# Performance work log

Measured on AMD Instinct MI355X. Metric: run time of the kernel, lower is better.

The kernel has to match this reference:

```python
import jax, jax.numpy as jnp
import numpy as np

B, S, D, F, E = 1, 1024, 1024, 4096, 8  # batch, seq, embed_dim, ffn_dim, num_experts(workers)
EPS = 1e-5


def setup_inputs() -> dict:
    key = jax.random.key(0)
    ks = jax.random.split(key, 4)
    x = jax.random.normal(ks[0], (B, S, D), jnp.float32)
    # expert centroids (orthogonal init gain 0.1 in original; scaled normal is fine for a reference)
    centroids = jax.random.normal(ks[1], (E, D), jnp.float32) * 0.1
    # per-expert BaseSublayer params (LayerNorm + ff1 + ff2); torch Linear convention W:[out,in]
    gamma = jnp.ones((E, D), jnp.float32)
    beta = jnp.zeros((E, D), jnp.float32)
    W1 = jax.random.normal(ks[2], (E, F, D), jnp.float32) * 0.02
    b1 = jnp.zeros((E, F), jnp.float32)
    W2 = jax.random.normal(ks[3], (E, D, F), jnp.float32) * 0.02  # zero-init in original; random for testing
    b2 = jnp.zeros((E, D), jnp.float32)
    return {"x": x, "centroids": centroids, "gamma": gamma, "beta": beta,
            "W1": W1, "b1": b1, "W2": W2, "b2": b2}


def _sublayer(xs, g, b, W1e, b1e, W2e, b2e):
    # BaseSublayer: xs + ff2(relu(ff1(LN(xs))))
    mu = jnp.mean(xs, axis=-1, keepdims=True)
    var = jnp.mean(jnp.square(xs - mu), axis=-1, keepdims=True)
    h = (xs - mu) * jax.lax.rsqrt(var + EPS) * g + b
    return xs + jax.nn.relu(h @ W1e.T + b1e) @ W2e.T + b2e


def reference(x, centroids, gamma, beta, W1, b1, W2, b2):
    feats = x.reshape(-1, x.shape[-1])                      # [T, D]
    # affinity matmul is under torch.no_grad in the original -> stop_gradient
    scores = jax.lax.stop_gradient(feats @ centroids.T)     # [T, E]
    expert = jnp.argmax(scores, axis=1)                     # greedy top-1 assignment
    onehot = jax.nn.one_hot(expert, E, dtype=feats.dtype)   # [T, E]
    # sigmoid gate: alpha = sigmoid(x . centroid[expert(x)])
    alpha = jax.nn.sigmoid(jnp.sum(feats * centroids[expert], axis=-1, keepdims=True))
    # run each expert's sublayer over all tokens, combine by assignment (dense reference
    # for the sort/gather dispatch + scatter combine of the original)
    ys = jax.vmap(_sublayer, in_axes=(None, 0, 0, 0, 0, 0, 0))(
        feats, gamma, beta, W1, b1, W2, b2)                 # [E, T, D]
    y = jnp.einsum('te,etd->td', onehot, ys)                # [T, D]
    out = alpha * y + (1.0 - alpha) * feats
    return out.reshape(x.shape)
```

## Files before the change

kernel.cpp:

```cpp
#include <hip/hip_runtime.h>
#include <hip/hip_bf16.h>

#define TOK 1024
#define DIM 1024
#define FF  4096
#define NE  8
#define EPSV 1e-5f
#define BUCKET_STRIDE 1040
#define MAXT 16
#define NKC 4
#define KC  (FF / NKC)

typedef __attribute__((ext_vector_type(8))) short short8;
typedef __attribute__((ext_vector_type(4))) float floatx4;

#define OFF_HNORM  0
#define OFF_H1     (OFF_HNORM + (size_t)TOK*DIM*2)
#define OFF_PART   (OFF_H1 + (size_t)TOK*FF*2)
#define OFF_ALPHA  (OFF_PART + (size_t)NKC*TOK*DIM*4)
#define OFF_EID    (OFF_ALPHA + TOK*4)
#define OFF_CNT    (OFF_EID + TOK*4)
#define OFF_NT     (OFF_CNT + NE*4)
#define OFF_TILES  (OFF_NT + 4)
#define OFF_BUCKET (OFF_TILES + 64*4)
#define OFF_FLAGS  (OFF_BUCKET + NE*BUCKET_STRIDE*4)

struct Ptr8 { const void* p[8]; };

__device__ __forceinline__ void gload16(const void* g, void* l) {
    __builtin_amdgcn_global_load_lds(
        (const __attribute__((address_space(1))) void*)g,
        (__attribute__((address_space(3))) void*)l, 16, 0, 0);
}

__device__ __forceinline__ float ldf(const void* p, size_t i, int f32) {
    if (f32) return ((const float*)p)[i];
    union { unsigned u; float f; } v;
    v.u = ((unsigned)((const unsigned short*)p)[i]) << 16;
    return v.f;
}

__device__ __forceinline__ short bf16rne(float f) {
    unsigned u = __float_as_uint(f);
    return (short)((u + 0x7FFFu + ((u >> 16) & 1u)) >> 16);
}

__device__ __forceinline__ void stout(void* p, size_t i, float v, int f32) {
    if (f32) ((float*)p)[i] = v;
    else ((__hip_bfloat16*)p)[i] = __float2bfloat16(v);
}

__global__ void k_init(Ptr8 ptrs, int* __restrict__ cnt, int* __restrict__ flags) {
    const int tid = threadIdx.x;
    if (tid < NE) cnt[tid] = 0;
    if (tid < 8) {
        const unsigned* w = (const unsigned*)ptrs.p[tid];
        int f32 = 0;
        for (int i = 0; i < 64; i++) {
            const unsigned v = w[i];
            if (v == 0x3F800000u) { f32 = 1; break; }
            const unsigned lo = v & 0xFFFFu;
            if (lo != 0) {
                const unsigned e = (lo >> 7) & 0xFFu;
                if (e < 0x60u || e > 0x9Fu) { f32 = 1; break; }
            }
        }
        flags[tid] = f32;
    }
    __syncthreads();
    if (tid == 0) {
        int o = 0;
        for (int i = 0; i < 8; i++) o |= flags[i];
        flags[8] = o;
    }
}

__global__ __launch_bounds__(256) void k_route_ln(
    const void* __restrict__ x,
    const void* __restrict__ cent,
    const void* __restrict__ gamma,
    const void* __restrict__ beta,
    const int* __restrict__ flags,
    __hip_bfloat16* __restrict__ hnorm,
    float* __restrict__ alpha,
    int* __restrict__ eid,
    int* __restrict__ cnt,
    int* __restrict__ bucket)
{
    __shared__ float centS[NE * DIM];
    __shared__ float part[4][10];
    __shared__ float bc[3];

    const int tid = threadIdx.x;
    const int t = blockIdx.x;
    const int fx = flags[0], fc = flags[1], fg = flags[2], fb = flags[3];

    for (int i = tid; i < NE * DIM; i += 256) centS[i] = ldf(cent, i, fc);

    float xv[4];
    #pragma unroll
    for (int i = 0; i < 4; i++)
        xv[i] = ldf(x, (size_t)t * DIM + tid + 256 * i, fx);

    __syncthreads();

    float s = 0.f, sq = 0.f, c[NE];
    #pragma unroll
    for (int e = 0; e < NE; e++) c[e] = 0.f;

    #pragma unroll
    for (int i = 0; i < 4; i++) {
        const int d = tid + 256 * i;
        const float f = xv[i];
        s += f; sq += f * f;
        #pragma unroll
        for (int e = 0; e < NE; e++)
            c[e] += f * centS[e * DIM + d];
    }

    #pragma unroll
    for (int o = 32; o > 0; o >>= 1) {
        s  += __shfl_xor(s, o);
        sq += __shfl_xor(sq, o);
        #pragma unroll
        for (int e = 0; e < NE; e++) c[e] += __shfl_xor(c[e], o);
    }
    const int wid = tid >> 6, lid = tid & 63;
    if (lid == 0) {
        part[wid][0] = s; part[wid][1] = sq;
        #pragma unroll
        for (int e = 0; e < NE; e++) part[wid][2 + e] = c[e];
    }
    __syncthreads();

    if (tid == 0) {
        float S = 0.f, SQ = 0.f, C[NE];
        #pragma unroll
        for (int e = 0; e < NE; e++) C[e] = 0.f;
        for (int w = 0; w < 4; w++) {
            S += part[w][0]; SQ += part[w][1];
            #pragma unroll
            for (int e = 0; e < NE; e++) C[e] += part[w][2 + e];
        }
        const float mu = S / (float)DIM;
        const float var = SQ / (float)DIM - mu * mu;
        const float rstd = rsqrtf(var + EPSV);
        int be = 0; float bs = C[0];
        #pragma unroll
        for (int e = 1; e < NE; e++)
            if (C[e] > bs) { bs = C[e]; be = e; }
        alpha[t] = 1.f / (1.f + expf(-bs));
        eid[t] = be;
        const int pos = atomicAdd(&cnt[be], 1);
        bucket[be * BUCKET_STRIDE + pos] = t;
        bc[0] = mu; bc[1] = rstd; bc[2] = __int_as_float(be);
    }
    __syncthreads();

    const float mu = bc[0], rstd = bc[1];
    const int e = __float_as_int(bc[2]);
    #pragma unroll
    for (int i = 0; i < 4; i++) {
        const int d = tid + 256 * i;
        const float g = ldf(gamma, (size_t)e * DIM + d, fg);
        const float b = ldf(beta,  (size_t)e * DIM + d, fb);
        const float h = (xv[i] - mu) * rstd * g + b;
        hnorm[(size_t)t * DIM + d] = __float2bfloat16(h);
    }
}

__global__ void k_plan(const int* __restrict__ cnt, int* __restrict__ bucket,
                       int* __restrict__ tiles, int* __restrict__ numTiles)
{
    if (threadIdx.x == 0 && blockIdx.x == 0) {
        int nt = 0;
        for (int e = 0; e < NE; e++) {
            const int n = cnt[e];
            const int mt = (n + 127) >> 7;
            const int fill = (n > 0) ? bucket[e * BUCKET_STRIDE] : 0;
            for (int i = n; i < mt * 128; i++) bucket[e * BUCKET_STRIDE + i] = fill;
            for (int i = 0; i < mt; i++) tiles[nt++] = (e << 16) | (i * 128);
        }
        *numTiles = nt;
    }
}

template<int FW>
__device__ __forceinline__ void stageB(const char* W, char* ldsbuf,
                                       int wid, int lane,
                                       long rowbase, long rowlen, int kbase)
{
    if (FW) {
        #pragma unroll
        for (int i = 0; i < 8; i++) {
            const int chunk = wid * 8 + i;
            const int row = chunk * 2 + (lane >> 5);
            const int p = lane & 31;
            const int col = (p ^ (row & 15)) << 2;
            const char* src = W + ((rowbase + row) * rowlen + kbase + col) * 4;
            gload16(src, ldsbuf + chunk * 1024);
        }
    } else {
        #pragma unroll
        for (int i = 0; i < 4; i++) {
            const int chunk = wid * 4 + i;
            const int row = chunk * 4 + (lane >> 4);
            const int p = lane & 15;
            const int col = (p ^ (row & 15)) << 3;
            const char* src = W + ((rowbase + row) * rowlen + kbase + col) * 2;
            gload16(src, ldsbuf + chunk * 1024);
        }
    }
}

template<int FW>
__device__ __forceinline__ short8 ldB(const char* ldsbuf, int row, int ks, int q) {
    if (FW) {
        const int s0 = ks * 8 + q * 2;
        const floatx4 f0 = *(const floatx4*)(ldsbuf + row * 512 + (((s0    ) ^ (row & 15)) << 4));
        const floatx4 f1 = *(const floatx4*)(ldsbuf + row * 512 + (((s0 + 1) ^ (row & 15)) << 4));
        short8 r;
        #pragma unroll
        for (int j = 0; j < 4; j++) { r[j] = bf16rne(f0[j]); r[4 + j] = bf16rne(f1[j]); }
        return r;
    } else {
        const int s = ks * 4 + q;
        return *(const short8*)(ldsbuf + row * 256 + ((s ^ (row & 15)) << 4));
    }
}

template<int FW>
__device__ __forceinline__ void ff1_core(
    const short* __restrict__ hnorm,
    const void* __restrict__ W1,
    const void* __restrict__ b1, const int fB,
    __hip_bfloat16* __restrict__ h1,
    const int* __restrict__ tiles, const int nt,
    const int* __restrict__ cnt, const int* __restrict__ bucket,
    char (*ldsB)[32768])
{
    const int bid = blockIdx.x;
    const int tile = bid >> 6;
    if (tile >= nt) return;
    const int nb = bid & 63;
    const int td = tiles[tile];
    const int e = td >> 16;
    const int mbase = td & 0xffff;
    const int ne = cnt[e];

    const int tid = threadIdx.x;
    const int wid = tid >> 6, lane = tid & 63;
    const int mr = lane & 15, q = lane >> 4;

    const int m0 = mbase + wid * 32;
    const int n0 = nb * 64;

    const short* Ap[2];
    #pragma unroll
    for (int am = 0; am < 2; am++) {
        const int tok = bucket[e * BUCKET_STRIDE + m0 + am * 16 + mr];
        Ap[am] = hnorm + (size_t)tok * DIM + q * 8;
    }

    floatx4 acc[2][4];
    #pragma unroll
    for (int am = 0; am < 2; am++)
        #pragma unroll
        for (int an = 0; an < 4; an++) acc[am][an] = (floatx4){0.f, 0.f, 0.f, 0.f};

    const long rowbase = (long)e * FF + n0;
    stageB<FW>((const char*)W1, ldsB[0], wid, lane, rowbase, DIM, 0);
    __syncthreads();

    int cur = 0;
    for (int kt = 0; kt < 8; kt++) {
        short8 Areg[4][2];
        #pragma unroll
        for (int ks = 0; ks < 4; ks++)
            #pragma unroll
            for (int am = 0; am < 2; am++)
                Areg[ks][am] = *(const short8*)(Ap[am] + kt * 128 + ks * 32);

        if (kt + 1 < 8)
            stageB<FW>((const char*)W1, ldsB[cur ^ 1], wid, lane, rowbase, DIM, (kt + 1) * 128);

        const char* lb = ldsB[cur];
        #pragma unroll
        for (int ks = 0; ks < 4; ks++) {
            short8 b[4];
            #pragma unroll
            for (int an = 0; an < 4; an++) b[an] = ldB<FW>(lb, an * 16 + mr, ks, q);
            #pragma unroll
            for (int am = 0; am < 2; am++)
                #pragma unroll
                for (int an = 0; an < 4; an++)
                    acc[am][an] = __builtin_amdgcn_mfma_f32_16x16x32_bf16(Areg[ks][am], b[an], acc[am][an], 0, 0, 0);
        }
        __syncthreads();
        cur ^= 1;
    }

    #pragma unroll
    for (int am = 0; am < 2; am++) {
        #pragma unroll
        for (int r = 0; r < 4; r++) {
            const int slot = m0 + am * 16 + q * 4 + r;
            if (slot < ne) {
                const int tr = bucket[e * BUCKET_STRIDE + slot];
                #pragma unroll
                for (int an = 0; an < 4; an++) {
                    const int f = n0 + an * 16 + mr;
                    float v = acc[am][an][r] + ldf(b1, (size_t)e * FF + f, fB);
                    v = v > 0.f ? v : 0.f;
                    h1[(size_t)tr * FF + f] = __float2bfloat16(v);
                }
            }
        }
    }
}

__global__ __launch_bounds__(256) void k_ff1(
    const __hip_bfloat16* __restrict__ hnorm,
    const void* __restrict__ W1,
    const void* __restrict__ b1,
    const int* __restrict__ flags,
    __hip_bfloat16* __restrict__ h1,
    const int* __restrict__ tiles,
    const int* __restrict__ numTiles,
    const int* __restrict__ cnt,
    const int* __restrict__ bucket)
{
    __shared__ char ldsB[2][32768];
    const int nt = *numTiles;
    if (flags[4]) ff1_core<1>((const short*)hnorm, W1, b1, flags[5], h1, tiles, nt, cnt, bucket, ldsB);
    else          ff1_core<0>((const short*)hnorm, W1, b1, flags[5], h1, tiles, nt, cnt, bucket, ldsB);
}

template<int FW>
__device__ __forceinline__ void ff2_core(
    const short* __restrict__ h1,
    const void* __restrict__ W2,
    float* __restrict__ part,
    const int* __restrict__ tiles, const int nt,
    const int* __restrict__ cnt, const int* __restrict__ bucket,
    char (*ldsB)[32768])
{
    const int bid = blockIdx.x;
    const int tile = bid >> 6;
    if (tile >= nt) return;
    const int nb = (bid >> 2) & 15;
    const int kc = bid & 3;
    const int td = tiles[tile];
    const int e = td >> 16;
    const int mbase = td & 0xffff;
    const int ne = cnt[e];

    const int tid = threadIdx.x;
    const int wid = tid >> 6, lane = tid & 63;
    const int mr = lane & 15, q = lane >> 4;

    const int m0 = mbase + wid * 32;
    const int n0 = nb * 64;
    const int kbase = kc * KC;

    const short* Ap[2];
    #pragma unroll
    for (int am = 0; am < 2; am++) {
        const int tok = bucket[e * BUCKET_STRIDE + m0 + am * 16 + mr];
        Ap[am] = h1 + (size_t)tok * FF + kbase + q * 8;
    }

    floatx4 acc[2][4];
    #pragma unroll
    for (int am = 0; am < 2; am++)
        #pragma unroll
        for (int an = 0; an < 4; an++) acc[am][an] = (floatx4){0.f, 0.f, 0.f, 0.f};

    const long rowbase = (long)e * DIM + n0;
    stageB<FW>((const char*)W2, ldsB[0], wid, lane, rowbase, FF, kbase);
    __syncthreads();

    int cur = 0;
    for (int kt = 0; kt < 8; kt++) {
        short8 Areg[4][2];
        #pragma unroll
        for (int ks = 0; ks < 4; ks++)
            #pragma unroll
            for (int am = 0; am < 2; am++)
                Areg[ks][am] = *(const short8*)(Ap[am] + kt * 128 + ks * 32);

        if (kt + 1 < 8)
            stageB<FW>((const char*)W2, ldsB[cur ^ 1], wid, lane, rowbase, FF, kbase + (kt + 1) * 128);

        const char* lb = ldsB[cur];
        #pragma unroll
        for (int ks = 0; ks < 4; ks++) {
            short8 b[4];
            #pragma unroll
            for (int an = 0; an < 4; an++) b[an] = ldB<FW>(lb, an * 16 + mr, ks, q);
            #pragma unroll
            for (int am = 0; am < 2; am++)
                #pragma unroll
                for (int an = 0; an < 4; an++)
                    acc[am][an] = __builtin_amdgcn_mfma_f32_16x16x32_bf16(Areg[ks][am], b[an], acc[am][an], 0, 0, 0);
        }
        __syncthreads();
        cur ^= 1;
    }

    float* pk = part + (size_t)kc * TOK * DIM;
    #pragma unroll
    for (int am = 0; am < 2; am++) {
        #pragma unroll
        for (int r = 0; r < 4; r++) {
            const int slot = m0 + am * 16 + q * 4 + r;
            if (slot < ne) {
                const int tr = bucket[e * BUCKET_STRIDE + slot];
                #pragma unroll
                for (int an = 0; an < 4; an++) {
                    const int d = n0 + an * 16 + mr;
                    pk[(size_t)tr * DIM + d] = acc[am][an][r];
                }
            }
        }
    }
}

__global__ __launch_bounds__(256) void k_ff2(
    const __hip_bfloat16* __restrict__ h1,
    const void* __restrict__ W2,
    const int* __restrict__ flags,
    float* __restrict__ part,
    const int* __restrict__ tiles,
    const int* __restrict__ numTiles,
    const int* __restrict__ cnt,
    const int* __restrict__ bucket)
{
    __shared__ char ldsB[2][32768];
    const int nt = *numTiles;
    if (flags[6]) ff2_core<1>((const short*)h1, W2, part, tiles, nt, cnt, bucket, ldsB);
    else          ff2_core<0>((const short*)h1, W2, part, tiles, nt, cnt, bucket, ldsB);
}

__global__ __launch_bounds__(256) void k_out(
    const float* __restrict__ part,
    const void* __restrict__ b2,
    const void* __restrict__ x,
    const int* __restrict__ flags,
    const float* __restrict__ alpha,
    const int* __restrict__ eid,
    void* __restrict__ out)
{
    const int t = blockIdx.x;
    const int tid = threadIdx.x;
    const int fB = flags[7], fx = flags[0], fo = flags[8];
    const int e = eid[t];
    const float al = alpha[t];
    const int d0 = tid * 4;

    floatx4 s = (floatx4){0.f, 0.f, 0.f, 0.f};
    #pragma unroll
    for (int kc = 0; kc < NKC; kc++) {
        const floatx4 p = *(const floatx4*)(part + (size_t)kc * TOK * DIM + (size_t)t * DIM + d0);
        s[0] += p[0]; s[1] += p[1]; s[2] += p[2]; s[3] += p[3];
    }
    #pragma unroll
    for (int j = 0; j < 4; j++) {
        const int d = d0 + j;
        const float xb = ldf(x, (size_t)t * DIM + d, fx);
        const float v = xb + al * (s[j] + ldf(b2, (size_t)e * DIM + d, fB));
        stout(out, (size_t)t * DIM + d, v, fo);
    }
}

extern "C" void kernel_launch(void* const* d_in, const int* in_sizes, int n_in,
                              void* d_out, int out_size, void* d_ws, size_t ws_size,
                              hipStream_t stream) {
    char* ws = (char*)d_ws;
    Ptr8 ptrs;
    for (int i = 0; i < 8; i++) ptrs.p[i] = d_in[i];

    __hip_bfloat16* hnorm = (__hip_bfloat16*)(ws + OFF_HNORM);
    __hip_bfloat16* h1    = (__hip_bfloat16*)(ws + OFF_H1);
    float* part           = (float*)(ws + OFF_PART);
    float* alpha          = (float*)(ws + OFF_ALPHA);
    int* eid              = (int*)(ws + OFF_EID);
    int* cnt              = (int*)(ws + OFF_CNT);
    int* numTiles         = (int*)(ws + OFF_NT);
    int* tiles            = (int*)(ws + OFF_TILES);
    int* bucket           = (int*)(ws + OFF_BUCKET);
    int* flags            = (int*)(ws + OFF_FLAGS);

    k_init<<<1, 64, 0, stream>>>(ptrs, cnt, flags);
    k_route_ln<<<TOK, 256, 0, stream>>>(d_in[0], d_in[1], d_in[2], d_in[3], flags,
                                        hnorm, alpha, eid, cnt, bucket);
    k_plan<<<1, 64, 0, stream>>>(cnt, bucket, tiles, numTiles);
    k_ff1<<<MAXT * 64, 256, 0, stream>>>(hnorm, d_in[4], d_in[5], flags, h1,
                                         tiles, numTiles, cnt, bucket);
    k_ff2<<<MAXT * 64, 256, 0, stream>>>(h1, d_in[6], flags, part,
                                         tiles, numTiles, cnt, bucket);
    k_out<<<TOK, 256, 0, stream>>>(part, d_in[7], d_in[0], flags, alpha, eid, d_out);
}
```

Before: 382.4 us.

## Stage weights through registers and store bf16 in LDS to halve LDS footprint

Replaces direct global-to-LDS async loads of weight tiles with register-staged loads that convert fp32 weights to bf16 once before writing them to LDS. The swizzled bf16 layout halves the LDS buffers from 64KB to 32KB per block and removes the repeated per-wave fp32-to-bf16 conversion inside the MFMA loop. Launch bounds now request 3 blocks per CU. The trade-off is extra registers to hold the in-flight tile and LDS writes that are no longer asynchronous, placed after the compute phase.

New measurement: 402.0 us. 1.05x slower.

```diff
diff --git a/kernel.cpp b/kernel.cpp
--- a/kernel.cpp
+++ b/kernel.cpp
@@ -10,6 +10,7 @@
 #define MAXT 16
 #define NKC 4
 #define KC  (FF / NKC)
+#define BK  128
 
 typedef __attribute__((ext_vector_type(8))) short short8;
 typedef __attribute__((ext_vector_type(4))) float floatx4;
@@ -26,12 +27,6 @@
 #define OFF_FLAGS  (OFF_BUCKET + NE*BUCKET_STRIDE*4)
 
 struct Ptr8 { const void* p[8]; };
-
-__device__ __forceinline__ void gload16(const void* g, void* l) {
-    __builtin_amdgcn_global_load_lds(
-        (const __attribute__((address_space(1))) void*)g,
-        (__attribute__((address_space(3))) void*)l, 16, 0, 0);
-}
 
 __device__ __forceinline__ float ldf(const void* p, size_t i, int f32) {
     if (f32) return ((const float*)p)[i];
@@ -185,48 +180,48 @@
     }
 }
 
+
 template<int FW>
-__device__ __forceinline__ void stageB(const char* W, char* ldsbuf,
-                                       int wid, int lane,
-                                       long rowbase, long rowlen, int kbase)
+__device__ __forceinline__ void stage_load(const char* W, long rowbase, long rowlen,
+                                           int kb, int row, int cg,
+                                           floatx4* wf, short8* wb)
 {
     if (FW) {
         #pragma unroll
-        for (int i = 0; i < 8; i++) {
-            const int chunk = wid * 8 + i;
-            const int row = chunk * 2 + (lane >> 5);
-            const int p = lane & 31;
-            const int col = (p ^ (row & 15)) << 2;
-            const char* src = W + ((rowbase + row) * rowlen + kbase + col) * 4;
-            gload16(src, ldsbuf + chunk * 1024);
-        }
+        for (int j2 = 0; j2 < 8; j2++)
+            wf[j2] = *(const floatx4*)(W + ((rowbase + row) * rowlen + kb + cg * 32 + j2 * 4) * 4);
     } else {
         #pragma unroll
-        for (int i = 0; i < 4; i++) {
-            const int chunk = wid * 4 + i;
-            const int row = chunk * 4 + (lane >> 4);
-            const int p = lane & 15;
-            const int col = (p ^ (row & 15)) << 3;
-            const char* src = W + ((rowbase + row) * rowlen + kbase + col) * 2;
-            gload16(src, ldsbuf + chunk * 1024);
-        }
+        for (int j = 0; j < 4; j++)
+            wb[j] = *(const short8*)(W + ((rowbase + row) * rowlen + kb + (cg * 4 + j) * 8) * 2);
     }
 }
 
 template<int FW>
-__device__ __forceinline__ short8 ldB(const char* ldsbuf, int row, int ks, int q) {
-    if (FW) {
-        const int s0 = ks * 8 + q * 2;
-        const floatx4 f0 = *(const floatx4*)(ldsbuf + row * 512 + (((s0    ) ^ (row & 15)) << 4));
-        const floatx4 f1 = *(const floatx4*)(ldsbuf + row * 512 + (((s0 + 1) ^ (row & 15)) << 4));
+__device__ __forceinline__ void stage_write(char* buf, int row, int cg,
+                                            const floatx4* wf, const short8* wb)
+{
+    char* dst = buf + row * 256;
+    #pragma unroll
+    for (int j = 0; j < 4; j++) {
         short8 r;
-        #pragma unroll
-        for (int j = 0; j < 4; j++) { r[j] = bf16rne(f0[j]); r[4 + j] = bf16rne(f1[j]); }
-        return r;
-    } else {
-        const int s = ks * 4 + q;
-        return *(const short8*)(ldsbuf + row * 256 + ((s ^ (row & 15)) << 4));
-    }
+        if (FW) {
+            const floatx4 f0 = wf[j * 2], f1 = wf[j * 2 + 1];
+            #pragma unroll
+            for (int jj = 0; jj < 4; jj++) {
+                r[jj]     = bf16rne(f0[jj]);
+                r[4 + jj] = bf16rne(f1[jj]);
+            }
+        } else {
+            r = wb[j];
+        }
+        *(short8*)(dst + (((cg * 4 + j) ^ (row & 15)) << 4)) = r;
+    }
+}
+
+__device__ __forceinline__ short8 ldB(const char* lb, int row, int ks, int q) {
+    const int s = ks * 4 + q;
+    return *(const short8*)(lb + row * 256 + ((s ^ (row & 15)) << 4));
 }
 
 template<int FW>
@@ -237,7 +232,7 @@
     __hip_bfloat16* __restrict__ h1,
     const int* __restrict__ tiles, const int nt,
     const int* __restrict__ cnt, const int* __restrict__ bucket,
-    char (*ldsB)[32768])
+    char (*ldsB)[16384])
 {
     const int bid = blockIdx.x;
     const int tile = bid >> 6;
@@ -251,6 +246,7 @@
     const int tid = threadIdx.x;
     const int wid = tid >> 6, lane = tid & 63;
     const int mr = lane & 15, q = lane >> 4;
+    const int row = tid >> 2, cg = tid & 3;
 
     const int m0 = mbase + wid * 32;
     const int n0 = nb * 64;
@@ -269,33 +265,39 @@
         for (int an = 0; an < 4; an++) acc[am][an] = (floatx4){0.f, 0.f, 0.f, 0.f};
 
     const long rowbase = (long)e * FF + n0;
-    stageB<FW>((const char*)W1, ldsB[0], wid, lane, rowbase, DIM, 0);
+
+    floatx4 wf[8]; short8 wb[4];
+    stage_load<FW>((const char*)W1, rowbase, DIM, 0, row, cg, wf, wb);
+    stage_write<FW>(ldsB[0], row, cg, wf, wb);
     __syncthreads();
 
     int cur = 0;
-    for (int kt = 0; kt < 8; kt++) {
+    for (int kt = 0; kt < DIM / BK; kt++) {
         short8 Areg[4][2];
         #pragma unroll
         for (int ks = 0; ks < 4; ks++)
             #pragma unroll
             for (int am = 0; am < 2; am++)
-                Areg[ks][am] = *(const short8*)(Ap[am] + kt * 128 + ks * 32);
-
-        if (kt + 1 < 8)
-            stageB<FW>((const char*)W1, ldsB[cur ^ 1], wid, lane, rowbase, DIM, (kt + 1) * 128);
+                Areg[ks][am] = *(const short8*)(Ap[am] + kt * BK + ks * 32);
+
+        if (kt + 1 < DIM / BK)
+            stage_load<FW>((const char*)W1, rowbase, DIM, (kt + 1) * BK, row, cg, wf, wb);
 
         const char* lb = ldsB[cur];
         #pragma unroll
         for (int ks = 0; ks < 4; ks++) {
             short8 b[4];
             #pragma unroll
-            for (int an = 0; an < 4; an++) b[an] = ldB<FW>(lb, an * 16 + mr, ks, q);
+            for (int an = 0; an < 4; an++) b[an] = ldB(lb, an * 16 + mr, ks, q);
             #pragma unroll
             for (int am = 0; am < 2; am++)
                 #pragma unroll
                 for (int an = 0; an < 4; an++)
                     acc[am][an] = __builtin_amdgcn_mfma_f32_16x16x32_bf16(Areg[ks][am], b[an], acc[am][an], 0, 0, 0);
         }
+
+        if (kt + 1 < DIM / BK)
+            stage_write<FW>(ldsB[cur ^ 1], row, cg, wf, wb);
         __syncthreads();
         cur ^= 1;
     }
@@ -319,7 +321,7 @@
     }
 }
 
-__global__ __launch_bounds__(256) void k_ff1(
+__global__ __launch_bounds__(256, 3) void k_ff1(
     const __hip_bfloat16* __restrict__ hnorm,
     const void* __restrict__ W1,
     const void* __restrict__ b1,
@@ -330,7 +332,7 @@
     const int* __restrict__ cnt,
     const int* __restrict__ bucket)
 {
-    __shared__ char ldsB[2][32768];
+    __shared__ char ldsB[2][16384];
     const int nt = *numTiles;
     if (flags[4]) ff1_core<1>((const short*)hnorm, W1, b1, flags[5], h1, tiles, nt, cnt, bucket, ldsB);
     else          ff1_core<0>((const short*)hnorm, W1, b1, flags[5], h1, tiles, nt, cnt, bucket, ldsB);
@@ -343,7 +345,7 @@
     float* __restrict__ part,
     const int* __restrict__ tiles, const int nt,
     const int* __restrict__ cnt, const int* __restrict__ bucket,
-    char (*ldsB)[32768])
+    char (*ldsB)[16384])
 {
     const int bid = blockIdx.x;
     const int tile = bid >> 6;
@@ -358,6 +360,7 @@
     const int tid = threadIdx.x;
     const int wid = tid >> 6, lane = tid & 63;
     const int mr = lane & 15, q = lane >> 4;
+    const int row = tid >> 2, cg = tid & 3;
 
     const int m0 = mbase + wid * 32;
     const int n0 = nb * 64;
@@ -377,33 +380,39 @@
         for (int an = 0; an < 4; an++) acc[am][an] = (floatx4){0.f, 0.f, 0.f, 0.f};
 
     const long rowbase = (long)e * DIM + n0;
-    stageB<FW>((const char*)W2, ldsB[0], wid, lane, rowbase, FF, kbase);
+
+    floatx4 wf[8]; short8 wb[4];
+    stage_load<FW>((const char*)W2, rowbase, FF, kbase, row, cg, wf, wb);
+    stage_write<FW>(ldsB[0], row, cg, wf, wb);
     __syncthreads();
 
     int cur = 0;
-    for (int kt = 0; kt < 8; kt++) {
+    for (int kt = 0; kt < KC / BK; kt++) {
         short8 Areg[4][2];
         #pragma unroll
         for (int ks = 0; ks < 4; ks++)
             #pragma unroll
             for (int am = 0; am < 2; am++)
-                Areg[ks][am] = *(const short8*)(Ap[am] + kt * 128 + ks * 32);
-
-        if (kt + 1 < 8)
-            stageB<FW>((const char*)W2, ldsB[cur ^ 1], wid, lane, rowbase, FF, kbase + (kt + 1) * 128);
+                Areg[ks][am] = *(const short8*)(Ap[am] + kt * BK + ks * 32);
+
+        if (kt + 1 < KC / BK)
+            stage_load<FW>((const char*)W2, rowbase, FF, kbase + (kt + 1) * BK, row, cg, wf, wb);
 
         const char* lb = ldsB[cur];
         #pragma unroll
         for (int ks = 0; ks < 4; ks++) {
             short8 b[4];
             #pragma unroll
-            for (int an = 0; an < 4; an++) b[an] = ldB<FW>(lb, an * 16 + mr, ks, q);
+            for (int an = 0; an < 4; an++) b[an] = ldB(lb, an * 16 + mr, ks, q);
             #pragma unroll
             for (int am = 0; am < 2; am++)
                 #pragma unroll
                 for (int an = 0; an < 4; an++)
                     acc[am][an] = __builtin_amdgcn_mfma_f32_16x16x32_bf16(Areg[ks][am], b[an], acc[am][an], 0, 0, 0);
         }
+
+        if (kt + 1 < KC / BK)
+            stage_write<FW>(ldsB[cur ^ 1], row, cg, wf, wb);
         __syncthreads();
         cur ^= 1;
     }
@@ -426,7 +435,7 @@
     }
 }
 
-__global__ __launch_bounds__(256) void k_ff2(
+__global__ __launch_bounds__(256, 3) void k_ff2(
     const __hip_bfloat16* __restrict__ h1,
     const void* __restrict__ W2,
     const int* __restrict__ flags,
@@ -436,7 +445,7 @@
     const int* __restrict__ cnt,
     const int* __restrict__ bucket)
 {
-    __shared__ char ldsB[2][32768];
+    __shared__ char ldsB[2][16384];
     const int nt = *numTiles;
     if (flags[6]) ff2_core<1>((const short*)h1, W2, part, tiles, nt, cnt, bucket, ldsB);
     else          ff2_core<0>((const short*)h1, W2, part, tiles, nt, cnt, bucket, ldsB);
```
